# Kernel optimization log

Hardware: AMD Instinct MI355X
Metric: run time of the kernel (lower is better)

Reference implementation:

```python
import jax, jax.numpy as jnp
import numpy as np

B, NE, NR, A = 512, 100000, 400, 256
ENT, REL, HIST = 200, 200, 400
ADIM = ENT + REL  # 400
HUGE = 1e31
EPS = 1e-20


def _linear(x, W, b):
    return x @ W.T + b


def setup_inputs() -> dict:
    key = jax.random.key(0)
    ks = jax.random.split(key, 26)
    w = lambda k, o, i: (jax.random.normal(k, (o, i)) * 0.02).astype(jnp.float32)
    bz = lambda o: jnp.zeros((o,), jnp.float32)
    inp = {}
    inp['H'] = jax.random.normal(ks[0], (B, HIST), jnp.float32)
    mask = (jax.random.uniform(ks[1], (B, A)) > 0.3).astype(jnp.float32)
    inp['action_mask'] = mask.at[:, 0].set(1.0)  # ensure at least one valid action
    inp['entity_emb'] = jax.random.normal(ks[2], (NE, ENT), jnp.float32) * 0.1
    inp['relation_emb'] = jax.random.normal(ks[3], (NR, REL), jnp.float32) * 0.1
    inp['W1'] = w(ks[4], ADIM, ENT + HIST + REL); inp['b1'] = bz(ADIM)
    inp['W2'] = w(ks[5], ADIM, ADIM); inp['b2'] = bz(ADIM)
    inp['W3'] = w(ks[6], REL, ENT); inp['b3'] = bz(REL)
    inp['W4'] = w(ks[7], REL, REL); inp['b4'] = bz(REL)
    inp['W5'] = w(ks[8], REL, REL + ENT); inp['b5'] = bz(REL)
    inp['W6'] = w(ks[9], REL, REL + REL); inp['b6'] = bz(REL)
    inp['Watt'] = w(ks[10], REL, ADIM + REL); inp['batt'] = bz(REL)
    inp['e'] = jax.random.randint(ks[11], (B,), 0, NE)
    inp['q'] = jax.random.randint(ks[12], (B,), 0, NR)
    inp['pred_id'] = jax.random.randint(ks[13], (B, 1), 0, NE)
    inp['r_space'] = jax.random.randint(ks[14], (B, A), 0, NR)
    inp['e_space'] = jax.random.randint(ks[15], (B, A), 0, NE)
    return inp


def reference(H, action_mask, entity_emb, relation_emb,
              W1, b1, W2, b2, W3, b3, W4, b4, W5, b5, W6, b6, Watt, batt,
              e, q, pred_id, r_space, e_space):
    # --- embed lookups ---
    Q = relation_emb[q]                 # [B, REL]
    E = entity_emb[e]                   # [B, ENT]
    # --- small MLP (dropout in eval mode -> identity) ---
    X = jax.nn.relu(_linear(jnp.concatenate([E, H, Q], -1), W1, b1))
    X2 = _linear(X, W2, b2)             # [B, ADIM]
    # --- full relation attention (multinomial sample replaced by given pred_id) ---
    pred_emb = entity_emb[pred_id]      # [B, 1, ENT]
    pred_ent_info = _linear(pred_emb, W3, b3)       # [B, 1, REL]
    relation_K = _linear(relation_emb, W4, b4)      # [NR, REL]
    local_att = jnp.einsum('bkd,rd->bkr', pred_ent_info, relation_K)  # [B,1,NR]
    beta = jnp.einsum('bkr,rd->bkd', jax.nn.softmax(local_att, -1), relation_emb).sum(1)  # [B, REL]
    # cat([R_all expand, pred_emb expand], -1).sum(1) == [sum_r R_all, NR * pred_emb]
    rel_sum = relation_emb.sum(0)                   # [REL]
    alpha_in = jnp.concatenate([jnp.broadcast_to(rel_sum, (H.shape[0], REL)),
                                NR * pred_emb[:, 0, :]], -1)
    alpha = _linear(alpha_in, W5, b5)               # [B, REL]
    V_A = _linear(jnp.concatenate([alpha, beta], -1), W6, b6)  # [B, REL]
    relation_att = jax.nn.softmax(
        _linear(jnp.concatenate([X2, V_A], -1), Watt, batt) @ relation_emb.T, -1)  # [B, NR]
    # --- policy_nn_fun: action embedding gather + masked softmax ---
    A_emb = jnp.concatenate([relation_emb[r_space], entity_emb[e_space]], -1)  # [B, A, ADIM]
    scores = jnp.einsum('bad,bd->ba', A_emb, X2) - (1.0 - action_mask) * HUGE
    action_dist = jax.nn.softmax(scores, -1)        # [B, A]
    entropy = -jnp.sum(action_dist * jnp.log(action_dist + EPS), -1)  # [B]
    return action_dist, entropy, relation_att
```

## Files before the change

kernel.cpp:

```cpp
#include <hip/hip_runtime.h>
#include <cstdint>
#include <cstddef>

#define BB 512
#define NEn 100000
#define NRr 400
#define AA 256
#define ENTd 200
#define RELd 200
#define HISTd 400
#define ADIMd 400

__device__ __forceinline__ float dot4(const float4 a, const float4 b) {
  return a.x * b.x + a.y * b.y + a.z * b.z + a.w * b.w;
}
__device__ __forceinline__ void fma4(float4& a, const float4 w, const float c) {
  a.x += w.x * c; a.y += w.y * c; a.z += w.z * c; a.w += w.w * c;
}
__device__ __forceinline__ float wave_rmax(float v) {
#pragma unroll
  for (int off = 32; off > 0; off >>= 1) v = fmaxf(v, __shfl_xor(v, off));
  return v;
}
__device__ __forceinline__ float wave_rsum(float v) {
#pragma unroll
  for (int off = 32; off > 0; off >>= 1) v += __shfl_xor(v, off);
  return v;
}

__global__ __launch_bounds__(256) void prep1_kernel(
    const float* __restrict__ rel_emb, const float* __restrict__ W4,
    const float* __restrict__ b4, const float* __restrict__ W5,
    const float* __restrict__ b5, const float* __restrict__ W6,
    const float* __restrict__ Watt, const float* __restrict__ W1,
    const float* __restrict__ W2, float* __restrict__ RK,
    float* __restrict__ P, float* __restrict__ W6bb, float* __restrict__ ab,
    float* __restrict__ relT, float* __restrict__ WaT,
    float* __restrict__ W1T, float* __restrict__ W2T) {
  int t = threadIdx.x;
  int blk = blockIdx.x;
  if (blk == 0) {
    __shared__ float rs[RELd];
    if (t < RELd) {
      float s = 0.f;
      for (int r = 0; r < NRr; r += 4) {
        s += rel_emb[(size_t)r * RELd + t] + rel_emb[(size_t)(r + 1) * RELd + t] +
             rel_emb[(size_t)(r + 2) * RELd + t] + rel_emb[(size_t)(r + 3) * RELd + t];
      }
      rs[t] = s;
    }
    __syncthreads();
    if (t < RELd) {
      float acc = b5[t];
      const float4* w = (const float4*)(W5 + (size_t)t * 400);
      const float4* rv = (const float4*)rs;
      for (int k = 0; k < 50; ++k) acc += dot4(w[k], rv[k]);
      ab[t] = acc;
    }
  } else if (blk <= 50) {
    int r0 = (blk - 1) * 8;
    __shared__ float re[8][RELd];
    for (int i = t; i < 8 * RELd; i += 256)
      re[i / RELd][i % RELd] = rel_emb[(size_t)(r0 + i / RELd) * RELd + i % RELd];
    __syncthreads();
    if (t < RELd) {
      float bv = b4[t];
      float acc[8];
#pragma unroll
      for (int s = 0; s < 8; ++s) acc[s] = bv;
      const float4* w = (const float4*)(W4 + (size_t)t * RELd);
      for (int k = 0; k < 50; ++k) {
        float4 wv = w[k];
#pragma unroll
        for (int s = 0; s < 8; ++s) acc[s] += dot4(wv, ((const float4*)re[s])[k]);
      }
#pragma unroll
      for (int s = 0; s < 8; ++s) RK[(size_t)(r0 + s) * RELd + t] = acc[s];
    }
  } else if (blk <= 75) {
    int i0 = (blk - 51) * 8;
    __shared__ float w6s[8][200];
    for (int i = t; i < 8 * 200; i += 256)
      w6s[i / 200][i % 200] = W6[(size_t)(i0 + i / 200) * 400 + i % 200];
    __syncthreads();
    if (t < 200) {
      int k = t;
      float acc[8] = {0, 0, 0, 0, 0, 0, 0, 0};
      for (int j = 0; j < 200; j += 4) {
        float r0v = W5[(size_t)j * 400 + 200 + k];
        float r1v = W5[(size_t)(j + 1) * 400 + 200 + k];
        float r2v = W5[(size_t)(j + 2) * 400 + 200 + k];
        float r3v = W5[(size_t)(j + 3) * 400 + 200 + k];
#pragma unroll
        for (int s = 0; s < 8; ++s)
          acc[s] += w6s[s][j] * r0v + w6s[s][j + 1] * r1v + w6s[s][j + 2] * r2v +
                    w6s[s][j + 3] * r3v;
      }
#pragma unroll
      for (int s = 0; s < 8; ++s) P[(size_t)(i0 + s) * 200 + k] = 400.f * acc[s];
    }
  } else if (blk <= 100) {
    int u0 = (blk - 76) * 8;
    __shared__ float wbs[8][200];
    for (int i = t; i < 8 * 200; i += 256)
      wbs[i / 200][i % 200] = Watt[(size_t)(u0 + i / 200) * 600 + 400 + i % 200];
    __syncthreads();
    if (t < 200) {
      int j = t;
      float acc[8] = {0, 0, 0, 0, 0, 0, 0, 0};
      for (int i = 0; i < 200; i += 4) {
        float r0v = W6[(size_t)i * 400 + 200 + j];
        float r1v = W6[(size_t)(i + 1) * 400 + 200 + j];
        float r2v = W6[(size_t)(i + 2) * 400 + 200 + j];
        float r3v = W6[(size_t)(i + 3) * 400 + 200 + j];
#pragma unroll
        for (int s = 0; s < 8; ++s)
          acc[s] += wbs[s][i] * r0v + wbs[s][i + 1] * r1v + wbs[s][i + 2] * r2v +
                    wbs[s][i + 3] * r3v;
      }
#pragma unroll
      for (int s = 0; s < 8; ++s) W6bb[(size_t)(u0 + s) * 200 + j] = acc[s];
    }
  } else {
    __shared__ float tlds[64][65];
    int tb = blk - 101;
    const float* src;
    float* dst;
    int M, N, LD, ti, tj;
    if (tb < 28) {
      src = rel_emb; dst = relT; M = 400; N = 200; LD = 200;
      ti = tb / 4; tj = tb % 4;
    } else if (tb < 56) {
      tb -= 28;
      src = Watt; dst = WaT; M = 200; N = 400; LD = 600;
      ti = tb / 7; tj = tb % 7;
    } else if (tb < 147) {
      tb -= 56;
      src = W1; dst = W1T; M = 400; N = 800; LD = 800;
      ti = tb / 13; tj = tb % 13;
    } else {
      tb -= 147;
      src = W2; dst = W2T; M = 400; N = 400; LD = 400;
      ti = tb / 7; tj = tb % 7;
    }
    int i0 = ti * 64, j0 = tj * 64;
    for (int idx = t; idx < 4096; idx += 256) {
      int r = idx >> 6, c = idx & 63;
      int i = i0 + r, j = j0 + c;
      if (i < M && j < N) tlds[r][c] = src[(size_t)i * LD + j];
    }
    __syncthreads();
    for (int idx = t; idx < 4096; idx += 256) {
      int r = idx >> 6, c = idx & 63;
      int j = j0 + r, i = i0 + c;
      if (i < M && j < N) dst[(size_t)j * M + i] = tlds[c][r];
    }
  }
}

__global__ __launch_bounds__(1024) void prep2_x1_kernel(
    const float* __restrict__ rel_emb, const float* __restrict__ W3,
    const float* __restrict__ b3, const float* __restrict__ W6,
    const float* __restrict__ Watt, const float* __restrict__ batt,
    const float* __restrict__ b6, const float* __restrict__ RK,
    const float* __restrict__ P, const float* __restrict__ W6bb,
    const float* __restrict__ ab, float* __restrict__ S_T,
    float* __restrict__ cvec, float* __restrict__ Q_T,
    float* __restrict__ REatt, float* __restrict__ v1,
    const float* __restrict__ ent_emb, const float* __restrict__ H,
    const int* __restrict__ e_idx, const int* __restrict__ q_idx,
    const float* __restrict__ W1T, const float* __restrict__ b1,
    float* __restrict__ X) {
  int t = threadIdx.x;
  int blk = blockIdx.x;
  if (blk < 50) {
    int r0 = blk * 8;
    __shared__ float rks[8][200];
    __shared__ float b3s[200];
    for (int i = t; i < 1600; i += 1024)
      rks[i / 200][i % 200] = RK[(size_t)r0 * 200 + i];
    if (t < 200) b3s[t] = b3[t];
    __syncthreads();
    if (t < 200) {
      int i = t;
      float acc[8] = {0, 0, 0, 0, 0, 0, 0, 0};
      for (int j = 0; j < 200; j += 4) {
        float w0 = W3[(size_t)j * 200 + i];
        float w1 = W3[(size_t)(j + 1) * 200 + i];
        float w2 = W3[(size_t)(j + 2) * 200 + i];
        float w3v = W3[(size_t)(j + 3) * 200 + i];
#pragma unroll
        for (int s = 0; s < 8; ++s)
          acc[s] += w0 * rks[s][j] + w1 * rks[s][j + 1] + w2 * rks[s][j + 2] +
                    w3v * rks[s][j + 3];
      }
      float4 s0 = make_float4(acc[0], acc[1], acc[2], acc[3]);
      float4 s1 = make_float4(acc[4], acc[5], acc[6], acc[7]);
      *(float4*)(S_T + (size_t)i * 400 + r0) = s0;
      *(float4*)(S_T + (size_t)i * 400 + r0 + 4) = s1;
    }
    if (t < 256) {
      int w = t >> 6, lane = t & 63;
      float p0 = 0.f, p1 = 0.f;
      for (int j = lane; j < 200; j += 64) {
        p0 += b3s[j] * rks[w][j];
        p1 += b3s[j] * rks[w + 4][j];
      }
      p0 = wave_rsum(p0);
      p1 = wave_rsum(p1);
      if (lane == 0) {
        cvec[r0 + w] = p0;
        cvec[r0 + w + 4] = p1;
      }
    }
  } else if (blk < 75) {
    int u0 = (blk - 50) * 8;
    __shared__ float wbs[8][200];
    for (int i = t; i < 1600; i += 1024)
      wbs[i / 200][i % 200] = Watt[(size_t)(u0 + i / 200) * 600 + 400 + i % 200];
    __syncthreads();
    if (t < 200) {
      int k = t;
      float acc[8] = {0, 0, 0, 0, 0, 0, 0, 0};
      for (int i = 0; i < 200; i += 4) {
        float r0v = P[(size_t)i * 200 + k];
        float r1v = P[(size_t)(i + 1) * 200 + k];
        float r2v = P[(size_t)(i + 2) * 200 + k];
        float r3v = P[(size_t)(i + 3) * 200 + k];
#pragma unroll
        for (int s = 0; s < 8; ++s)
          acc[s] += wbs[s][i] * r0v + wbs[s][i + 1] * r1v + wbs[s][i + 2] * r2v +
                    wbs[s][i + 3] * r3v;
      }
      float4 s0 = make_float4(acc[0], acc[1], acc[2], acc[3]);
      float4 s1 = make_float4(acc[4], acc[5], acc[6], acc[7]);
      *(float4*)(Q_T + (size_t)k * 200 + u0) = s0;
      *(float4*)(Q_T + (size_t)k * 200 + u0 + 4) = s1;
    }
  } else if (blk < 125) {
    int r0 = (blk - 75) * 8;
    __shared__ float rels[8][200];
    for (int i = t; i < 1600; i += 1024)
      rels[i / 200][i % 200] = rel_emb[(size_t)r0 * 200 + i];
    __syncthreads();
    if (t < 200) {
      float acc[8] = {0, 0, 0, 0, 0, 0, 0, 0};
      const float4* w = (const float4*)(W6bb + (size_t)t * 200);
      for (int k = 0; k < 50; ++k) {
        float4 wv = w[k];
#pragma unroll
        for (int s = 0; s < 8; ++s) acc[s] += dot4(wv, ((const float4*)rels[s])[k]);
      }
#pragma unroll
      for (int s = 0; s < 8; ++s) REatt[(size_t)(r0 + s) * 200 + t] = acc[s];
    }
  } else if (blk == 125) {
    __shared__ float abs_[200];
    __shared__ float us[200];
    if (t < 200) abs_[t] = ab[t];
    __syncthreads();
    if (t < 200) {
      float u = b6[t];
      const float4* w = (const float4*)(W6 + (size_t)t * 400);
      const float4* rv = (const float4*)abs_;
      for (int k = 0; k < 50; ++k) u += dot4(w[k], rv[k]);
      us[t] = u;
    }
    __syncthreads();
    if (t < 200) {
      float v = batt[t];
      const float4* w = (const float4*)(Watt + (size_t)t * 600 + 400);
      const float4* rv = (const float4*)us;
      for (int k = 0; k < 50; ++k) v += dot4(w[k], rv[k]);
      v1[t] = v;
    }
  } else {
    int b0 = (blk - 126) * 2;
    __shared__ float cv[2][800];
    __shared__ float prt[6400];
    for (int i = t; i < 1600; i += 1024) {
      int s = i / 800, k = i % 800;
      float v;
      if (k < ENTd)
        v = ent_emb[(size_t)e_idx[b0 + s] * ENTd + k];
      else if (k < ENTd + HISTd)
        v = H[(size_t)(b0 + s) * HISTd + (k - ENTd)];
      else
        v = rel_emb[(size_t)q_idx[b0 + s] * RELd + (k - ENTd - HISTd)];
      cv[s][k] = v;
    }
    __syncthreads();
    if (t < 800) {
      int g = t % 100, h = t / 100;
      float4 accA = make_float4(0, 0, 0, 0);
      float4 accB = make_float4(0, 0, 0, 0);
      const float4* wp = ((const float4*)W1T) + g;
      int k0 = h * 100;
#pragma unroll 4
      for (int kk = 0; kk < 100; ++kk) {
        int k = k0 + kk;
        float4 wv = wp[(size_t)k * 100];
        fma4(accA, wv, cv[0][k]);
        fma4(accB, wv, cv[1][k]);
      }
      ((float4*)prt)[(h * 2 + 0) * 100 + g] = accA;
      ((float4*)prt)[(h * 2 + 1) * 100 + g] = accB;
    }
    __syncthreads();
    if (t < 800) {
      int s = t / 400, j = t % 400;
      float a = b1[j];
#pragma unroll
      for (int h = 0; h < 8; ++h) a += prt[(h * 2 + s) * 400 + j];
      X[(size_t)(b0 + s) * ADIMd + j] = fmaxf(a, 0.f);
    }
  }
}

__global__ __launch_bounds__(1024) void x2rx_kernel(
    const float* __restrict__ X, const float* __restrict__ W2T,
    const float* __restrict__ b2, const float* __restrict__ relT,
    float* __restrict__ X2, float* __restrict__ RX) {
  int b0 = blockIdx.x * 2;
  int t = threadIdx.x;
  __shared__ float cv[2][400];
  __shared__ float prt[6400];
  __shared__ float x2lo[2][200];
  for (int i = t; i < 800; i += 1024) cv[i / 400][i % 400] = X[(size_t)b0 * 400 + i];
  __syncthreads();
  if (t < 800) {
    int g = t % 100, h = t / 100;
    float4 accA = make_float4(0, 0, 0, 0);
    float4 accB = make_float4(0, 0, 0, 0);
    const float4* wp = ((const float4*)W2T) + g;
    int k0 = h * 50;
#pragma unroll 4
    for (int kk = 0; kk < 50; ++kk) {
      int k = k0 + kk;
      float4 wv = wp[(size_t)k * 100];
      fma4(accA, wv, cv[0][k]);
      fma4(accB, wv, cv[1][k]);
    }
    ((float4*)prt)[(h * 2 + 0) * 100 + g] = accA;
    ((float4*)prt)[(h * 2 + 1) * 100 + g] = accB;
  }
  __syncthreads();
  if (t < 800) {
    int s = t / 400, j = t % 400;
    float a = b2[j];
#pragma unroll
    for (int h = 0; h < 8; ++h) a += prt[(h * 2 + s) * 400 + j];
    X2[(size_t)(b0 + s) * ADIMd + j] = a;
    if (j < 200) x2lo[s][j] = a;
  }
  __syncthreads();
  if (t < 800) {
    int g = t % 100, h = t / 100;
    float4 accA = make_float4(0, 0, 0, 0);
    float4 accB = make_float4(0, 0, 0, 0);
    const float4* rp = ((const float4*)relT) + g;
    int k0 = h * 25;
#pragma unroll 4
    for (int kk = 0; kk < 25; ++kk) {
      int k = k0 + kk;
      float4 wv = rp[(size_t)k * 100];
      fma4(accA, wv, x2lo[0][k]);
      fma4(accB, wv, x2lo[1][k]);
    }
    ((float4*)prt)[(h * 2 + 0) * 100 + g] = accA;
    ((float4*)prt)[(h * 2 + 1) * 100 + g] = accB;
  }
  __syncthreads();
  if (t < 800) {
    int s = t / 400, r = t % 400;
    float a = 0.f;
#pragma unroll
    for (int h = 0; h < 8; ++h) a += prt[(h * 2 + s) * 400 + r];
    RX[(size_t)(b0 + s) * NRr + r] = a;
  }
}

__global__ __launch_bounds__(1024) void tail_kernel(
    const float* __restrict__ ent_emb, const int* __restrict__ pred_id,
    const float* __restrict__ X2, const float* __restrict__ S_T,
    const float* __restrict__ cvec, const float* __restrict__ Q_T,
    const float* __restrict__ REatt, const float* __restrict__ relT,
    const float* __restrict__ WaT, const float* __restrict__ v1c,
    const float* __restrict__ RX, const int* __restrict__ r_space,
    const int* __restrict__ e_space, const float* __restrict__ mask,
    float* __restrict__ out_ratt, float* __restrict__ out_dist,
    float* __restrict__ out_ent) {
  int t = threadIdx.x;
  int w = t >> 6, lane = t & 63;
  __shared__ float pes[2][200];
  __shared__ float x2s[2][400];
  __shared__ float pp[2][400];
  __shared__ float av[2][200];
  __shared__ float prt[6400];
  __shared__ float wred[2][8];
  __shared__ float x2hi[200];
  __shared__ float scl[256];
  __shared__ float wr[4];

  if (blockIdx.x < 256) {
    int b0 = blockIdx.x * 2;
    for (int i = t; i < 1200; i += 1024) {
      if (i < 400)
        pes[i / 200][i % 200] =
            ent_emb[(size_t)pred_id[b0 + i / 200] * ENTd + i % 200];
      else {
        int k = i - 400;
        x2s[k / 400][k % 400] = X2[(size_t)b0 * 400 + k];
      }
    }
    __syncthreads();
    if (t < 800) {
      int g = t % 100, h = t / 100;
      float4 accA = make_float4(0, 0, 0, 0);
      float4 accB = make_float4(0, 0, 0, 0);
      const float4* sp = ((const float4*)S_T) + g;
      int k0 = h * 25;
#pragma unroll 5
      for (int kk = 0; kk < 25; ++kk) {
        int k = k0 + kk;
        float4 wv = sp[(size_t)k * 100];
        fma4(accA, wv, pes[0][k]);
        fma4(accB, wv, pes[1][k]);
      }
      ((float4*)prt)[(h * 2 + 0) * 100 + g] = accA;
      ((float4*)prt)[(h * 2 + 1) * 100 + g] = accB;
    }
    __syncthreads();
    if (t < 800) {
      int s = t / 400, r = t % 400;
      float a = cvec[r];
#pragma unroll
      for (int h = 0; h < 8; ++h) a += prt[(h * 2 + s) * 400 + r];
      pp[s][r] = a;
    }
    __syncthreads();
    int row = w >> 3, q = w & 7;
    {
      int r = q * 64 + lane;
      float m = (r < 400) ? pp[row][r] : -INFINITY;
      m = wave_rmax(m);
      if (lane == 0) wred[row][q] = m;
      __syncthreads();
      float gm = wred[row][0];
#pragma unroll
      for (int i = 1; i < 8; ++i) gm = fmaxf(gm, wred[row][i]);
      __syncthreads();
      float e = 0.f;
      if (r < 400) {
        e = expf(pp[row][r] - gm);
        pp[row][r] = e;
      }
      float sum = wave_rsum(e);
      if (lane == 0) wred[row][q] = sum;
      __syncthreads();
      float gs = 0.f;
#pragma unroll
      for (int i = 0; i < 8; ++i) gs += wred[row][i];
      float inv = 1.f / gs;
      if (r < 400) pp[row][r] *= inv;
    }
    __syncthreads();
    if (t < 800) {
      int g = t % 50, h = t / 50;
      float4 accA, accB;
      if (h == 0) {
        accA = ((const float4*)v1c)[g];
        accB = accA;
      } else {
        accA = make_float4(0, 0, 0, 0);
        accB = make_float4(0, 0, 0, 0);
      }
      {
        const float4* wp = ((const float4*)WaT) + g;
        int k0 = h * 25;
#pragma unroll 5
        for (int kk = 0; kk < 25; ++kk) {
          int k = k0 + kk;
          float4 wv = wp[(size_t)k * 50];
          fma4(accA, wv, x2s[0][k]);
          fma4(accB, wv, x2s[1][k]);
        }
      }
      if (h < 8) {
        const float4* qp = ((const float4*)Q_T) + g;
        int k0 = h * 25;
#pragma unroll 5
        for (int kk = 0; kk < 25; ++kk) {
          int k = k0 + kk;
          float4 wv = qp[(size_t)k * 50];
          fma4(accA, wv, pes[0][k]);
          fma4(accB, wv, pes[1][k]);
        }
      }
      {
        const float4* rp = ((const float4*)REatt) + g;
        int r0 = h * 25;
#pragma unroll 5
        for (int kk = 0; kk < 25; ++kk) {
          int r = r0 + kk;
          float4 wv = rp[(size_t)r * 50];
          fma4(accA, wv, pp[0][r]);
          fma4(accB, wv, pp[1][r]);
        }
      }
      ((float4*)prt)[(h * 2 + 0) * 50 + g] = accA;
      ((float4*)prt)[(h * 2 + 1) * 50 + g] = accB;
    }
    __syncthreads();
    if (t < 400) {
      int s = t / 200, j = t % 200;
      float a = 0.f;
#pragma unroll
      for (int h = 0; h < 16; ++h) a += prt[(h * 2 + s) * 200 + j];
      av[s][j] = a;
    }
    __syncthreads();
    if (t < 800) {
      int g = t % 100, h = t / 100;
      float4 accA = make_float4(0, 0, 0, 0);
      float4 accB = make_float4(0, 0, 0, 0);
      const float4* rp = ((const float4*)relT) + g;
      int k0 = h * 25;
#pragma unroll 5
      for (int kk = 0; kk < 25; ++kk) {
        int k = k0 + kk;
        float4 wv = rp[(size_t)k * 100];
        fma4(accA, wv, av[0][k]);
        fma4(accB, wv, av[1][k]);
      }
      ((float4*)prt)[(h * 2 + 0) * 100 + g] = accA;
      ((float4*)prt)[(h * 2 + 1) * 100 + g] = accB;
    }
    __syncthreads();
    if (t < 800) {
      int s = t / 400, r = t % 400;
      float a = 0.f;
#pragma unroll
      for (int h = 0; h < 8; ++h) a += prt[(h * 2 + s) * 400 + r];
      pp[s][r] = a;
    }
    __syncthreads();
    {
      int r = q * 64 + lane;
      float m = (r < 400) ? pp[row][r] : -INFINITY;
      m = wave_rmax(m);
      if (lane == 0) wred[row][q] = m;
      __syncthreads();
      float gm = wred[row][0];
#pragma unroll
      for (int i = 1; i < 8; ++i) gm = fmaxf(gm, wred[row][i]);
      __syncthreads();
      float e = 0.f;
      if (r < 400) e = expf(pp[row][r] - gm);
      float sum = wave_rsum(e);
      if (lane == 0) wred[row][q] = sum;
      __syncthreads();
      float gs = 0.f;
#pragma unroll
      for (int i = 0; i < 8; ++i) gs += wred[row][i];
      float inv = 1.f / gs;
      if (r < 400) out_ratt[(size_t)(b0 + row) * 400 + r] = e * inv;
    }
  } else {
    int b = blockIdx.x - 256;
    if (t >= 200 && t < 400) x2hi[t - 200] = X2[(size_t)b * ADIMd + t];
    __syncthreads();
    const float4* xh = (const float4*)x2hi;
    for (int c = 0; c < 2; ++c) {
      int abase = w * 16 + c * 8;
      int ei[8];
#pragma unroll
      for (int u = 0; u < 8; ++u) ei[u] = e_space[(size_t)b * AA + abase + u];
      float p[8];
      if (lane < 50) {
        float4 xv = xh[lane];
#pragma unroll
        for (int u = 0; u < 8; ++u) {
          float4 vv = ((const float4*)(ent_emb + (size_t)ei[u] * ENTd))[lane];
          p[u] = dot4(vv, xv);
        }
      } else {
#pragma unroll
        for (int u = 0; u < 8; ++u) p[u] = 0.f;
      }
#pragma unroll
      for (int off = 32; off > 0; off >>= 1) {
#pragma unroll
        for (int u = 0; u < 8; ++u) p[u] += __shfl_xor(p[u], off);
      }
      if (lane == 0) {
#pragma unroll
        for (int u = 0; u < 8; ++u) scl[abase + u] = p[u];
      }
    }
    __syncthreads();
    float sc = -INFINITY;
    if (t < 256) {
      int r = r_space[(size_t)b * AA + t];
      sc = scl[t] + RX[(size_t)b * NRr + r] -
           (1.f - mask[(size_t)b * AA + t]) * 1e31f;
    }
    __syncthreads();
    if (w < 4) {
      float m = wave_rmax(sc);
      if (lane == 0) wr[w] = m;
    }
    __syncthreads();
    float gm = fmaxf(fmaxf(wr[0], wr[1]), fmaxf(wr[2], wr[3]));
    float e = (t < 256) ? expf(sc - gm) : 0.f;
    __syncthreads();
    if (w < 4) {
      float s2 = wave_rsum(e);
      if (lane == 0) wr[w] = s2;
    }
    __syncthreads();
    float gs = wr[0] + wr[1] + wr[2] + wr[3];
    float p = e / gs;
    if (t < 256) out_dist[(size_t)b * AA + t] = p;
    float ent = (t < 256) ? -p * logf(p + 1e-20f) : 0.f;
    __syncthreads();
    if (w < 4) {
      float s3 = wave_rsum(ent);
      if (lane == 0) wr[w] = s3;
    }
    __syncthreads();
    if (t == 0) out_ent[b] = wr[0] + wr[1] + wr[2] + wr[3];
  }
}

extern "C" void kernel_launch(void* const* d_in, const int* in_sizes, int n_in,
                              void* d_out, int out_size, void* d_ws,
                              size_t ws_size, hipStream_t stream) {
  const float* H = (const float*)d_in[0];
  const float* mask = (const float*)d_in[1];
  const float* ent_emb = (const float*)d_in[2];
  const float* rel_emb = (const float*)d_in[3];
  const float* W1 = (const float*)d_in[4];
  const float* b1 = (const float*)d_in[5];
  const float* W2 = (const float*)d_in[6];
  const float* b2 = (const float*)d_in[7];
  const float* W3 = (const float*)d_in[8];
  const float* b3 = (const float*)d_in[9];
  const float* W4 = (const float*)d_in[10];
  const float* b4 = (const float*)d_in[11];
  const float* W5 = (const float*)d_in[12];
  const float* b5 = (const float*)d_in[13];
  const float* W6 = (const float*)d_in[14];
  const float* b6 = (const float*)d_in[15];
  const float* Watt = (const float*)d_in[16];
  const float* batt = (const float*)d_in[17];
  const int* e_idx = (const int*)d_in[18];
  const int* q_idx = (const int*)d_in[19];
  const int* pred_id = (const int*)d_in[20];
  const int* r_space = (const int*)d_in[21];
  const int* e_space = (const int*)d_in[22];

  float* ws = (float*)d_ws;
  float* RK = ws;
  float* S_T = ws + 80000;
  float* cvec = ws + 160000;
  float* P = ws + 160512;
  float* Q_T = ws + 200512;
  float* W6bb = ws + 240512;
  float* REatt = ws + 280512;
  float* relT = ws + 360512;
  float* WaT = ws + 440512;
  float* W1T = ws + 520512;
  float* W2T = ws + 840512;
  float* ab = ws + 1000512;
  float* v1 = ws + 1000768;
  float* X = ws + 1001024;
  float* X2 = ws + 1205824;
  float* RX = ws + 1410624;

  float* out = (float*)d_out;
  float* out_dist = out;
  float* out_ent = out + BB * AA;
  float* out_ratt = out + BB * AA + BB;

  hipLaunchKernelGGL(prep1_kernel, dim3(297), dim3(256), 0, stream, rel_emb,
                     W4, b4, W5, b5, W6, Watt, W1, W2, RK, P, W6bb, ab, relT,
                     WaT, W1T, W2T);
  hipLaunchKernelGGL(prep2_x1_kernel, dim3(382), dim3(1024), 0, stream,
                     rel_emb, W3, b3, W6, Watt, batt, b6, RK, P, W6bb, ab,
                     S_T, cvec, Q_T, REatt, v1, ent_emb, H, e_idx, q_idx,
                     W1T, b1, X);
  hipLaunchKernelGGL(x2rx_kernel, dim3(256), dim3(1024), 0, stream, X, W2T,
                     b2, relT, X2, RX);
  hipLaunchKernelGGL(tail_kernel, dim3(768), dim3(1024), 0, stream, ent_emb,
                     pred_id, X2, S_T, cvec, Q_T, REatt, relT, WaT, v1, RX,
                     r_space, e_space, mask, out_ratt, out_dist, out_ent);
}
```

Baseline: 101.9 us.

## Process four rows per X1 block, interleave tail block types, widen gather batch

In the first MLP layer each block now handles four batch rows instead of two, so every W1T weight load feeds four accumulators and the grid shrinks from 382 to 254 blocks. This halves the number of times W1T is streamed from memory, at the cost of more registers and twice the shared memory for the partial sums. The tail kernel now interleaves its attention blocks with the action-scoring blocks (one attention block per three) so the heavy and light block types mix across CUs instead of running in sequence. The entity-gather loop issues all sixteen row loads per wave at once instead of two batches of eight, exposing more memory-level parallelism while using more registers.

```diff
diff --git a/kernel.cpp b/kernel.cpp
--- a/kernel.cpp
+++ b/kernel.cpp
@@ -275,10 +275,10 @@
       v1[t] = v;
     }
   } else {
-    int b0 = (blk - 126) * 2;
-    __shared__ float cv[2][800];
-    __shared__ float prt[6400];
-    for (int i = t; i < 1600; i += 1024) {
+    int b0 = (blk - 126) * 4;
+    __shared__ float cv[4][800];
+    __shared__ float prt[12800];
+    for (int i = t; i < 3200; i += 1024) {
       int s = i / 800, k = i % 800;
       float v;
       if (k < ENTd)
@@ -292,26 +292,28 @@
     __syncthreads();
     if (t < 800) {
       int g = t % 100, h = t / 100;
-      float4 accA = make_float4(0, 0, 0, 0);
-      float4 accB = make_float4(0, 0, 0, 0);
+      float4 acc[4];
+#pragma unroll
+      for (int s = 0; s < 4; ++s) acc[s] = make_float4(0, 0, 0, 0);
       const float4* wp = ((const float4*)W1T) + g;
       int k0 = h * 100;
 #pragma unroll 4
       for (int kk = 0; kk < 100; ++kk) {
         int k = k0 + kk;
         float4 wv = wp[(size_t)k * 100];
-        fma4(accA, wv, cv[0][k]);
-        fma4(accB, wv, cv[1][k]);
-      }
-      ((float4*)prt)[(h * 2 + 0) * 100 + g] = accA;
-      ((float4*)prt)[(h * 2 + 1) * 100 + g] = accB;
-    }
-    __syncthreads();
-    if (t < 800) {
-      int s = t / 400, j = t % 400;
+#pragma unroll
+        for (int s = 0; s < 4; ++s) fma4(acc[s], wv, cv[s][k]);
+      }
+#pragma unroll
+      for (int s = 0; s < 4; ++s)
+        ((float4*)prt)[(h * 4 + s) * 100 + g] = acc[s];
+    }
+    __syncthreads();
+    for (int i = t; i < 1600; i += 1024) {
+      int s = i / 400, j = i % 400;
       float a = b1[j];
 #pragma unroll
-      for (int h = 0; h < 8; ++h) a += prt[(h * 2 + s) * 400 + j];
+      for (int h = 0; h < 8; ++h) a += prt[(h * 4 + s) * 400 + j];
       X[(size_t)(b0 + s) * ADIMd + j] = fmaxf(a, 0.f);
     }
   }
@@ -392,6 +394,7 @@
     float* __restrict__ out_ent) {
   int t = threadIdx.x;
   int w = t >> 6, lane = t & 63;
+  int g = blockIdx.x;
   __shared__ float pes[2][200];
   __shared__ float x2s[2][400];
   __shared__ float pp[2][400];
@@ -402,8 +405,8 @@
   __shared__ float scl[256];
   __shared__ float wr[4];
 
-  if (blockIdx.x < 256) {
-    int b0 = blockIdx.x * 2;
+  if (g % 3 == 0) {
+    int b0 = (g / 3) * 2;
     for (int i = t; i < 1200; i += 1024) {
       if (i < 400)
         pes[i / 200][i % 200] =
@@ -415,10 +418,10 @@
     }
     __syncthreads();
     if (t < 800) {
-      int g = t % 100, h = t / 100;
+      int gg = t % 100, h = t / 100;
       float4 accA = make_float4(0, 0, 0, 0);
       float4 accB = make_float4(0, 0, 0, 0);
-      const float4* sp = ((const float4*)S_T) + g;
+      const float4* sp = ((const float4*)S_T) + gg;
       int k0 = h * 25;
 #pragma unroll 5
       for (int kk = 0; kk < 25; ++kk) {
@@ -427,8 +430,8 @@
         fma4(accA, wv, pes[0][k]);
         fma4(accB, wv, pes[1][k]);
       }
-      ((float4*)prt)[(h * 2 + 0) * 100 + g] = accA;
-      ((float4*)prt)[(h * 2 + 1) * 100 + g] = accB;
+      ((float4*)prt)[(h * 2 + 0) * 100 + gg] = accA;
+      ((float4*)prt)[(h * 2 + 1) * 100 + gg] = accB;
     }
     __syncthreads();
     if (t < 800) {
@@ -466,17 +469,17 @@
     }
     __syncthreads();
     if (t < 800) {
-      int g = t % 50, h = t / 50;
+      int gg = t % 50, h = t / 50;
       float4 accA, accB;
       if (h == 0) {
-        accA = ((const float4*)v1c)[g];
+        accA = ((const float4*)v1c)[gg];
         accB = accA;
       } else {
         accA = make_float4(0, 0, 0, 0);
         accB = make_float4(0, 0, 0, 0);
       }
       {
-        const float4* wp = ((const float4*)WaT) + g;
+        const float4* wp = ((const float4*)WaT) + gg;
         int k0 = h * 25;
 #pragma unroll 5
         for (int kk = 0; kk < 25; ++kk) {
@@ -487,7 +490,7 @@
         }
       }
       if (h < 8) {
-        const float4* qp = ((const float4*)Q_T) + g;
+        const float4* qp = ((const float4*)Q_T) + gg;
         int k0 = h * 25;
 #pragma unroll 5
         for (int kk = 0; kk < 25; ++kk) {
@@ -498,7 +501,7 @@
         }
       }
       {
-        const float4* rp = ((const float4*)REatt) + g;
+        const float4* rp = ((const float4*)REatt) + gg;
         int r0 = h * 25;
 #pragma unroll 5
         for (int kk = 0; kk < 25; ++kk) {
@@ -508,8 +511,8 @@
           fma4(accB, wv, pp[1][r]);
         }
       }
-      ((float4*)prt)[(h * 2 + 0) * 50 + g] = accA;
-      ((float4*)prt)[(h * 2 + 1) * 50 + g] = accB;
+      ((float4*)prt)[(h * 2 + 0) * 50 + gg] = accA;
+      ((float4*)prt)[(h * 2 + 1) * 50 + gg] = accB;
     }
     __syncthreads();
     if (t < 400) {
@@ -521,10 +524,10 @@
     }
     __syncthreads();
     if (t < 800) {
-      int g = t % 100, h = t / 100;
+      int gg = t % 100, h = t / 100;
       float4 accA = make_float4(0, 0, 0, 0);
       float4 accB = make_float4(0, 0, 0, 0);
-      const float4* rp = ((const float4*)relT) + g;
+      const float4* rp = ((const float4*)relT) + gg;
       int k0 = h * 25;
 #pragma unroll 5
       for (int kk = 0; kk < 25; ++kk) {
@@ -533,8 +536,8 @@
         fma4(accA, wv, av[0][k]);
         fma4(accB, wv, av[1][k]);
       }
-      ((float4*)prt)[(h * 2 + 0) * 100 + g] = accA;
-      ((float4*)prt)[(h * 2 + 1) * 100 + g] = accB;
+      ((float4*)prt)[(h * 2 + 0) * 100 + gg] = accA;
+      ((float4*)prt)[(h * 2 + 1) * 100 + gg] = accB;
     }
     __syncthreads();
     if (t < 800) {
@@ -567,35 +570,35 @@
       if (r < 400) out_ratt[(size_t)(b0 + row) * 400 + r] = e * inv;
     }
   } else {
-    int b = blockIdx.x - 256;
+    int b = g - g / 3 - 1;
     if (t >= 200 && t < 400) x2hi[t - 200] = X2[(size_t)b * ADIMd + t];
     __syncthreads();
     const float4* xh = (const float4*)x2hi;
-    for (int c = 0; c < 2; ++c) {
-      int abase = w * 16 + c * 8;
-      int ei[8];
-#pragma unroll
-      for (int u = 0; u < 8; ++u) ei[u] = e_space[(size_t)b * AA + abase + u];
-      float p[8];
+    {
+      int abase = w * 16;
+      int ei[16];
+#pragma unroll
+      for (int u = 0; u < 16; ++u) ei[u] = e_space[(size_t)b * AA + abase + u];
+      float p[16];
       if (lane < 50) {
         float4 xv = xh[lane];
 #pragma unroll
-        for (int u = 0; u < 8; ++u) {
+        for (int u = 0; u < 16; ++u) {
           float4 vv = ((const float4*)(ent_emb + (size_t)ei[u] * ENTd))[lane];
           p[u] = dot4(vv, xv);
         }
       } else {
 #pragma unroll
-        for (int u = 0; u < 8; ++u) p[u] = 0.f;
+        for (int u = 0; u < 16; ++u) p[u] = 0.f;
       }
 #pragma unroll
       for (int off = 32; off > 0; off >>= 1) {
 #pragma unroll
-        for (int u = 0; u < 8; ++u) p[u] += __shfl_xor(p[u], off);
+        for (int u = 0; u < 16; ++u) p[u] += __shfl_xor(p[u], off);
       }
       if (lane == 0) {
 #pragma unroll
-        for (int u = 0; u < 8; ++u) scl[abase + u] = p[u];
+        for (int u = 0; u < 16; ++u) scl[abase + u] = p[u];
       }
     }
     __syncthreads();
@@ -686,7 +689,7 @@
   hipLaunchKernelGGL(prep1_kernel, dim3(297), dim3(256), 0, stream, rel_emb,
                      W4, b4, W5, b5, W6, Watt, W1, W2, RK, P, W6bb, ab, relT,
                      WaT, W1T, W2T);
-  hipLaunchKernelGGL(prep2_x1_kernel, dim3(382), dim3(1024), 0, stream,
+  hipLaunchKernelGGL(prep2_x1_kernel, dim3(254), dim3(1024), 0, stream,
                      rel_emb, W3, b3, W6, Watt, batt, b6, RK, P, W6bb, ab,
                      S_T, cvec, Q_T, REatt, v1, ent_emb, H, e_idx, q_idx,
                      W1T, b1, X);
```

Measured after the change: 109.1 us. +7.1%, slower.
